# Performance work log

Measured on AMD Instinct MI355X. Metric: run time of the kernel, lower is better.

The kernel has to match this reference:

```python
import jax, jax.numpy as jnp
import numpy as np
from math import sqrt

DIM = 256
HEADS = 4
GROUPS = min(DIM // 4, 32)  # = 32
EPS = 1e-6


def setup_inputs() -> dict:
    key = jax.random.key(0)
    ks = jax.random.split(key, 10)
    B, C, H, W = 16, DIM, 32, 32
    x = jax.random.normal(ks[0], (B, C, H, W), dtype=jnp.float32)
    s = 1.0 / sqrt(C)
    inp = {
        'x': x,
        'gn_scale': jnp.ones((C,), jnp.float32),
        'gn_bias': jnp.zeros((C,), jnp.float32),
        'Wq': jax.random.normal(ks[1], (C, C), jnp.float32) * s,
        'bq': jnp.zeros((C,), jnp.float32),
        'Wk': jax.random.normal(ks[2], (C, C), jnp.float32) * s,
        'bk': jnp.zeros((C,), jnp.float32),
        'Wv': jax.random.normal(ks[3], (C, C), jnp.float32) * s,
        'bv': jnp.zeros((C,), jnp.float32),
        'Wp': jax.random.normal(ks[4], (C, C), jnp.float32) * s,
        'bp': jnp.zeros((C,), jnp.float32),
    }
    return inp


def _group_norm(x, scale, bias):
    B, C, H, W = x.shape
    xg = x.reshape(B, GROUPS, C // GROUPS, H, W)
    mean = xg.mean(axis=(2, 3, 4), keepdims=True)
    var = xg.var(axis=(2, 3, 4), keepdims=True)
    xg = (xg - mean) * jax.lax.rsqrt(var + EPS)
    x = xg.reshape(B, C, H, W)
    return x * scale[None, :, None, None] + bias[None, :, None, None]


def _lin_ch(x, W, b):
    # 1x1 conv / linear over channel dim: (B,C,H,W) x (C,Cout) -> (B,Cout,H,W)
    return jnp.einsum('bchw,cd->bdhw', x, W) + b[None, :, None, None]


def reference(x, gn_scale, gn_bias, Wq, bq, Wk, bk, Wv, bv, Wp, bp):
    B, C, H, W = x.shape
    dh = C // HEADS
    _x = _group_norm(x, gn_scale, gn_bias)
    q = _lin_ch(_x, Wq, bq).reshape(B, HEADS, dh, H, W)
    k = _lin_ch(_x, Wk, bk).reshape(B, HEADS, dh, H, W)
    v = _lin_ch(_x, Wv, bv).reshape(B, HEADS, dh, H, W)
    scores = jnp.einsum('bhdxy,bhdij->bhxyij', q, k) / sqrt(C)
    scores = scores.reshape(B, HEADS, H, W, H * W)
    weights = jax.nn.softmax(scores, axis=-1).reshape(B, HEADS, H, W, H, W)
    h = jnp.einsum('bhxyij,bhdij->bhdxy', weights, v).reshape(B, C, H, W)
    h = _lin_ch(h, Wp, bp)
    ret = (x + h) / sqrt(2.0)
    return ret
```

## Files before the change

### kernel.cpp

```cpp
#include <hip/hip_runtime.h>
#include <hip/hip_bf16.h>

#define BATCH 16
#define CH    256
#define HW    1024
#define NH    4
#define DH    64
#define NG    32
#define CPG   8
#define EPSV  1e-6f

#define QSCALE 0.090168440055558706f

typedef __bf16 bf16x8 __attribute__((ext_vector_type(8)));
typedef float  f32x4  __attribute__((ext_vector_type(4)));

__device__ __forceinline__ unsigned short f2bf(float f) {
    union { __hip_bfloat16 h; unsigned short u; } cv;
    cv.h = __float2bfloat16(f);
    return cv.u;
}

__device__ __forceinline__ unsigned int fbits(float f) {
    union { float f; unsigned int u; } cv; cv.f = f; return cv.u;
}

__device__ __forceinline__ void gld_lds16(const unsigned short* g, unsigned short* l) {
    __builtin_amdgcn_global_load_lds(
        (const __attribute__((address_space(1))) void*)g,
        (__attribute__((address_space(3))) void*)l, 16, 0, 0);
}

__global__ void prep_kernel(const float* Wq, const float* Wk, const float* Wv,
                            const float* Wp, const float* bq, const float* bk,
                            const float* bv, unsigned short* wqkv_t,
                            unsigned short* wp_t, float* bqkv) {
    int idx = blockIdx.x * 256 + threadIdx.x;
    if (idx < 768 * 256) {
        int n = idx >> 8, c = idx & 255;
        const float* W = (n < 256) ? Wq : (n < 512) ? Wk : Wv;
        int d = n & 255;
        wqkv_t[idx] = f2bf(W[c * 256 + d]);
    } else if (idx < 768 * 256 + 256 * 256) {
        int j = idx - 768 * 256;
        int n = j >> 8, c = j & 255;
        wp_t[j] = f2bf(Wp[c * 256 + n]);
    }
    if (idx < 768)
        bqkv[idx] = (idx < 256) ? bq[idx] : (idx < 512) ? bk[idx - 256] : bv[idx - 512];
}

__global__ void gn_stats_kernel(const float* x, const float* scale, const float* bias,
                                float* coefA, float* coefB) {
    int bg = blockIdx.x;
    const float4* p = reinterpret_cast<const float4*>(x + (size_t)bg * (CPG * HW));
    int t = threadIdx.x;
    float s = 0.f, ss = 0.f;
    for (int i = t; i < CPG * HW / 4; i += 256) {
        float4 v = p[i];
        s += v.x + v.y + v.z + v.w;
        ss += v.x * v.x + v.y * v.y + v.z * v.z + v.w * v.w;
    }
    for (int o = 32; o; o >>= 1) { s += __shfl_down(s, o); ss += __shfl_down(ss, o); }
    __shared__ float as[4], ass[4];
    int w = t >> 6;
    if ((t & 63) == 0) { as[w] = s; ass[w] = ss; }
    __syncthreads();
    if (t < 8) {
        float S = as[0] + as[1] + as[2] + as[3];
        float SS = ass[0] + ass[1] + ass[2] + ass[3];
        float mean = S / (float)(CPG * HW);
        float var = SS / (float)(CPG * HW) - mean * mean;
        float rstd = rsqrtf(var + EPSV);
        int b = bg >> 5, g = bg & 31;
        int c = g * CPG + t;
        float a = rstd * scale[c];
        coefA[b * CH + c] = a;
        coefB[b * CH + c] = bias[c] - mean * a;
    }
}

__global__ __launch_bounds__(256) void qkv_kernel(const float* x,
        const float* coefA, const float* coefB,
        const unsigned short* wqkv_t, const float* bqkv,
        unsigned short* qb, unsigned short* kb, unsigned short* vb) {
    int t = threadIdx.x;
    int wv = t >> 6, lane = t & 63, quad = lane >> 4, ln = lane & 15;
    int wr = wv >> 1, wc = wv & 1;
    int bx = blockIdx.x;
    int m0 = bx * 128 + wr * 64;
    int n0 = blockIdx.y * 128 + wc * 64;
    int bb = bx >> 3;
    int p0 = (bx & 7) * 128;

    __shared__ __align__(16) unsigned short lds_a[128][40];

    const float* xb = x + (size_t)bb * CH * HW + p0;
    const float* cA = coefA + bb * CH;
    const float* cB = coefB + bb * CH;

    int sp = t & 127;
    int sbase = (t >> 7) * 2;

    f32x4 acc[4][4] = {};
    for (int k0 = 0; k0 < CH; k0 += 32) {
        bf16x8 wpk[2];
#pragma unroll
        for (int rep = 0; rep < 2; rep++) {
            int s = sbase + rep;
            int cb = k0 + s * 8;
            union { bf16x8 v8; __hip_bfloat162 h2[4]; } u;
#pragma unroll
            for (int j = 0; j < 4; j++) {
                float v0 = fmaf(xb[(size_t)(cb + 2 * j)     * HW + sp], cA[cb + 2 * j],     cB[cb + 2 * j]);
                float v1 = fmaf(xb[(size_t)(cb + 2 * j + 1) * HW + sp], cA[cb + 2 * j + 1], cB[cb + 2 * j + 1]);
                u.h2[j] = __float22bfloat162_rn(float2{v0, v1});
            }
            wpk[rep] = u.v8;
        }
        __syncthreads();
#pragma unroll
        for (int rep = 0; rep < 2; rep++) {
            int s = sbase + rep;
            int phys = s ^ (sp & 3);
            *reinterpret_cast<bf16x8*>(&lds_a[sp][phys * 8]) = wpk[rep];
        }
        __syncthreads();
        bf16x8 af[4], bfr[4];
#pragma unroll
        for (int i = 0; i < 4; i++) {
            int p = wr * 64 + i * 16 + ln;
            af[i] = *reinterpret_cast<const bf16x8*>(&lds_a[p][(quad ^ (p & 3)) * 8]);
        }
#pragma unroll
        for (int j = 0; j < 4; j++)
            bfr[j] = *reinterpret_cast<const bf16x8*>(
                wqkv_t + (size_t)(n0 + j * 16 + ln) * CH + k0 + quad * 8);
#pragma unroll
        for (int i = 0; i < 4; i++)
#pragma unroll
            for (int j = 0; j < 4; j++)
                acc[i][j] = __builtin_amdgcn_mfma_f32_16x16x32_bf16(af[i], bfr[j], acc[i][j], 0, 0, 0);
    }
#pragma unroll
    for (int j = 0; j < 4; j++) {
        int n = n0 + j * 16 + ln;
        float bias = bqkv[n];
        int which = n >> 8;
        int dh_ = n & 255;
        int head = dh_ >> 6, d = dh_ & 63;
#pragma unroll
        for (int i = 0; i < 4; i++) {
            int mb = m0 + i * 16 + quad * 4;
            int bi = mb >> 10, p = mb & 1023;
            int bh = bi * NH + head;
            if (which < 2) {
                unsigned short* dst = (which == 0 ? qb : kb) + (size_t)bh * HW * DH;
                float sc = (which == 0) ? QSCALE : 1.0f;
#pragma unroll
                for (int r = 0; r < 4; r++)
                    dst[(size_t)(p + r) * DH + d] = f2bf((acc[i][j][r] + bias) * sc);
            } else {
                unsigned short* dst = vb + ((size_t)bh * DH + d) * HW + p;
                ushort4 pk4;
                pk4.x = f2bf(acc[i][j][0] + bias);
                pk4.y = f2bf(acc[i][j][1] + bias);
                pk4.z = f2bf(acc[i][j][2] + bias);
                pk4.w = f2bf(acc[i][j][3] + bias);
                *reinterpret_cast<ushort4*>(dst) = pk4;
            }
        }
    }
}

__global__ __launch_bounds__(256) void attn_kernel(const unsigned short* qb,
        const unsigned short* kb, const unsigned short* vb, unsigned short* h_t) {
    int qblk = blockIdx.x, bh = blockIdx.y;
    int t = threadIdx.x;
    int wv = t >> 6, lane = t & 63, quad = lane >> 4, ln = lane & 15;
    int q0 = qblk * 128 + wv * 32;

    const unsigned short* Q = qb + (size_t)bh * HW * DH;
    const unsigned short* K = kb + (size_t)bh * HW * DH;
    const unsigned short* V = vb + (size_t)bh * DH * HW;

    __shared__ __align__(16) unsigned short kbuf[2][4096];
    __shared__ __align__(16) unsigned short vbuf[2][4096];
    __shared__ __align__(16) unsigned short pbuf[4][2][16][72];

    int c_a = wv * 64 + lane;
    int c_b = 256 + wv * 64 + lane;
    int pa = c_a >> 3, ja = (c_a & 7) ^ (pa & 7);
    int pb = c_b >> 3, jb = (c_b & 7) ^ (pb & 7);
    const unsigned short* pka = K + (size_t)pa * DH + ja * 8;
    const unsigned short* pkb = K + (size_t)pb * DH + jb * 8;
    const unsigned short* pva = V + (size_t)pa * HW + ja * 8;
    const unsigned short* pvb = V + (size_t)pb * HW + jb * 8;
    int lofs_a = wv * 512, lofs_b = 2048 + wv * 512;

    int koffs[4][2];
#pragma unroll
    for (int mt = 0; mt < 4; mt++) {
        int p = mt * 16 + ln, sw = p & 7;
#pragma unroll
        for (int kk = 0; kk < 2; kk++)
            koffs[mt][kk] = p * 64 + (((kk * 4 + quad) ^ sw) * 8);
    }

    bf16x8 qf[2][2];
#pragma unroll
    for (int nq = 0; nq < 2; nq++)
#pragma unroll
        for (int kk = 0; kk < 2; kk++)
            qf[nq][kk] = *reinterpret_cast<const bf16x8*>(
                Q + (size_t)(q0 + nq * 16 + ln) * DH + kk * 32 + quad * 8);

    f32x4 ls[2] = {};
    f32x4 o[2][4] = {};

    gld_lds16(pka, &kbuf[0][lofs_a]);
    gld_lds16(pkb, &kbuf[0][lofs_b]);
    gld_lds16(pva, &vbuf[0][lofs_a]);
    gld_lds16(pvb, &vbuf[0][lofs_b]);
    pka += 64 * DH; pkb += 64 * DH; pva += 64; pvb += 64;

#define ATTN_TILE(B, DO_STAGE)                                                      \
    {                                                                               \
        __syncthreads();                                                            \
        if (DO_STAGE) {                                                             \
            gld_lds16(pka, &kbuf[B ^ 1][lofs_a]);                                   \
            gld_lds16(pkb, &kbuf[B ^ 1][lofs_b]);                                   \
            gld_lds16(pva, &vbuf[B ^ 1][lofs_a]);                                   \
            gld_lds16(pvb, &vbuf[B ^ 1][lofs_b]);                                   \
            pka += 64 * DH; pkb += 64 * DH; pva += 64; pvb += 64;                   \
        }                                                                           \
        bf16x8 kf[4][2], vf[4][2];                                                  \
        _Pragma("unroll")                                                           \
        for (int mt = 0; mt < 4; mt++) {                                            \
            _Pragma("unroll")                                                       \
            for (int kk = 0; kk < 2; kk++) {                                        \
                kf[mt][kk] = *reinterpret_cast<const bf16x8*>(&kbuf[B][koffs[mt][kk]]); \
                vf[mt][kk] = *reinterpret_cast<const bf16x8*>(&vbuf[B][koffs[mt][kk]]); \
            }                                                                       \
        }                                                                           \
        f32x4 s[2][4] = {};                                                         \
        _Pragma("unroll")                                                           \
        for (int nq = 0; nq < 2; nq++)                                              \
            _Pragma("unroll")                                                       \
            for (int mt = 0; mt < 4; mt++) {                                        \
                s[nq][mt] = __builtin_amdgcn_mfma_f32_16x16x32_bf16(kf[mt][0], qf[nq][0], s[nq][mt], 0, 0, 0); \
                s[nq][mt] = __builtin_amdgcn_mfma_f32_16x16x32_bf16(kf[mt][1], qf[nq][1], s[nq][mt], 0, 0, 0); \
            }                                                                       \
        _Pragma("unroll")                                                           \
        for (int nq = 0; nq < 2; nq++)                                              \
            _Pragma("unroll")                                                       \
            for (int mt = 0; mt < 4; mt++) {                                        \
                float e0 = __builtin_amdgcn_exp2f(s[nq][mt][0]);                    \
                float e1 = __builtin_amdgcn_exp2f(s[nq][mt][1]);                    \
                float e2 = __builtin_amdgcn_exp2f(s[nq][mt][2]);                    \
                float e3 = __builtin_amdgcn_exp2f(s[nq][mt][3]);                    \
                ls[nq][0] += e0; ls[nq][1] += e1;                                   \
                ls[nq][2] += e2; ls[nq][3] += e3;                                   \
                uint2 pk2;                                                          \
                pk2.x = __builtin_amdgcn_perm(fbits(e1), fbits(e0), 0x07060302u);   \
                pk2.y = __builtin_amdgcn_perm(fbits(e3), fbits(e2), 0x07060302u);   \
                *reinterpret_cast<uint2*>(&pbuf[wv][nq][ln][mt * 16 + quad * 4]) = pk2; \
            }                                                                       \
        _Pragma("unroll")                                                           \
        for (int nq = 0; nq < 2; nq++)                                              \
            _Pragma("unroll")                                                       \
            for (int kk = 0; kk < 2; kk++) {                                        \
                bf16x8 pf = *reinterpret_cast<const bf16x8*>(&pbuf[wv][nq][ln][kk * 32 + quad * 8]); \
                _Pragma("unroll")                                                   \
                for (int mt = 0; mt < 4; mt++)                                      \
                    o[nq][mt] = __builtin_amdgcn_mfma_f32_16x16x32_bf16(vf[mt][kk], pf, o[nq][mt], 0, 0, 0); \
            }                                                                       \
    }

    for (int u = 0; u < 8; u++) {
        ATTN_TILE(0, true)
        ATTN_TILE(1, (u < 7))
    }
#undef ATTN_TILE

    int b_ = bh >> 2, head = bh & 3;
#pragma unroll
    for (int nq = 0; nq < 2; nq++) {
        float lsum = ls[nq][0] + ls[nq][1] + ls[nq][2] + ls[nq][3];
        lsum += __shfl_xor(lsum, 16);
        lsum += __shfl_xor(lsum, 32);
        float inv = 1.0f / lsum;
        unsigned short* dst = h_t + ((size_t)b_ * HW + q0 + nq * 16 + ln) * CH + head * DH;
#pragma unroll
        for (int mt = 0; mt < 4; mt++) {
            ushort4 pk4;
            pk4.x = f2bf(o[nq][mt][0] * inv);
            pk4.y = f2bf(o[nq][mt][1] * inv);
            pk4.z = f2bf(o[nq][mt][2] * inv);
            pk4.w = f2bf(o[nq][mt][3] * inv);
            *reinterpret_cast<ushort4*>(dst + mt * 16 + quad * 4) = pk4;
        }
    }
}

__global__ __launch_bounds__(256) void proj_kernel(const unsigned short* h_t,
        const unsigned short* wp_t, const float* bp, const float* x, float* out) {
    int t = threadIdx.x;
    int wv = t >> 6, lane = t & 63, quad = lane >> 4, ln = lane & 15;
    int wr = wv >> 1, wc = wv & 1;
    int m0 = blockIdx.x * 64 + wr * 32;
    int n0 = blockIdx.y * 128 + wc * 64;

    f32x4 acc[2][4] = {};
    for (int k0 = 0; k0 < CH; k0 += 32) {
        int koff = k0 + quad * 8;
        bf16x8 af[2], bfr[4];
#pragma unroll
        for (int i = 0; i < 2; i++)
            af[i] = *reinterpret_cast<const bf16x8*>(h_t + (size_t)(m0 + i * 16 + ln) * CH + koff);
#pragma unroll
        for (int j = 0; j < 4; j++)
            bfr[j] = *reinterpret_cast<const bf16x8*>(wp_t + (size_t)(n0 + j * 16 + ln) * CH + koff);
#pragma unroll
        for (int i = 0; i < 2; i++)
#pragma unroll
            for (int j = 0; j < 4; j++)
                acc[i][j] = __builtin_amdgcn_mfma_f32_16x16x32_bf16(af[i], bfr[j], acc[i][j], 0, 0, 0);
    }
    const float inv_s2 = 0.70710678118654752440f;
#pragma unroll
    for (int j = 0; j < 4; j++) {
        int n = n0 + j * 16 + ln;
        float bias = bp[n];
#pragma unroll
        for (int i = 0; i < 2; i++) {
            int mb = m0 + i * 16 + quad * 4;
            int bi = mb >> 10, p = mb & 1023;
            size_t off = ((size_t)(bi * CH + n)) * HW + p;
            float4 xv = *reinterpret_cast<const float4*>(x + off);
            float4 ov;
            ov.x = (xv.x + acc[i][j][0] + bias) * inv_s2;
            ov.y = (xv.y + acc[i][j][1] + bias) * inv_s2;
            ov.z = (xv.z + acc[i][j][2] + bias) * inv_s2;
            ov.w = (xv.w + acc[i][j][3] + bias) * inv_s2;
            *reinterpret_cast<float4*>(out + off) = ov;
        }
    }
}

extern "C" void kernel_launch(void* const* d_in, const int* in_sizes, int n_in,
                              void* d_out, int out_size, void* d_ws, size_t ws_size,
                              hipStream_t stream) {
    const float* x        = (const float*)d_in[0];
    const float* gn_scale = (const float*)d_in[1];
    const float* gn_bias  = (const float*)d_in[2];
    const float* Wq = (const float*)d_in[3];
    const float* bq = (const float*)d_in[4];
    const float* Wk = (const float*)d_in[5];
    const float* bk = (const float*)d_in[6];
    const float* Wv = (const float*)d_in[7];
    const float* bv = (const float*)d_in[8];
    const float* Wp = (const float*)d_in[9];
    const float* bp = (const float*)d_in[10];
    float* out = (float*)d_out;

    char* ws = (char*)d_ws;
    float*          bqkv   = (float*)(ws + 0);
    float*          coefA  = (float*)(ws + 4096);
    float*          coefB  = (float*)(ws + 20480);
    unsigned short* wqkv_t = (unsigned short*)(ws + 36864);
    unsigned short* wp_t   = (unsigned short*)(ws + 430080);
    unsigned short* h_t    = (unsigned short*)(ws + 1048576);
    unsigned short* qb     = (unsigned short*)(ws + 9437184);
    unsigned short* kb     = (unsigned short*)(ws + 17825792);
    unsigned short* vb     = (unsigned short*)(ws + 26214400);

    prep_kernel<<<1024, 256, 0, stream>>>(Wq, Wk, Wv, Wp, bq, bk, bv, wqkv_t, wp_t, bqkv);
    gn_stats_kernel<<<512, 256, 0, stream>>>(x, gn_scale, gn_bias, coefA, coefB);
    qkv_kernel<<<dim3(128, 6), 256, 0, stream>>>(x, coefA, coefB, wqkv_t, bqkv, qb, kb, vb);
    attn_kernel<<<dim3(8, 64), 256, 0, stream>>>(qb, kb, vb, h_t);
    proj_kernel<<<dim3(256, 2), 256, 0, stream>>>(h_t, wp_t, bp, x, out);
}
```

Before: 163.0 us.

## Merge prep and GN-stats kernels, retile QKV GEMM with prefetch, add MFMA priority

Folds the weight-conversion and group-norm statistics kernels into a single launch to save one kernel launch. Retiles the QKV GEMM to 64x256 block tiles, where each thread stages one 8-channel slot and prefetches the next slice of x into registers, with launch bounds requesting 3 blocks per SIMD. Wraps the attention MFMA sections in s_setprio so matrix-core work gets issue priority. The mix trades register pressure and smaller M tiles for fewer launches and better latency hiding.

After: 172.9 us. 6.0% more time.

```diff
diff --git a/kernel.cpp b/kernel.cpp
--- a/kernel.cpp
+++ b/kernel.cpp
@@ -31,56 +31,57 @@
         (__attribute__((address_space(3))) void*)l, 16, 0, 0);
 }
 
-__global__ void prep_kernel(const float* Wq, const float* Wk, const float* Wv,
-                            const float* Wp, const float* bq, const float* bk,
-                            const float* bv, unsigned short* wqkv_t,
-                            unsigned short* wp_t, float* bqkv) {
-    int idx = blockIdx.x * 256 + threadIdx.x;
-    if (idx < 768 * 256) {
-        int n = idx >> 8, c = idx & 255;
-        const float* W = (n < 256) ? Wq : (n < 512) ? Wk : Wv;
-        int d = n & 255;
-        wqkv_t[idx] = f2bf(W[c * 256 + d]);
-    } else if (idx < 768 * 256 + 256 * 256) {
-        int j = idx - 768 * 256;
-        int n = j >> 8, c = j & 255;
-        wp_t[j] = f2bf(Wp[c * 256 + n]);
-    }
-    if (idx < 768)
-        bqkv[idx] = (idx < 256) ? bq[idx] : (idx < 512) ? bk[idx - 256] : bv[idx - 512];
-}
-
-__global__ void gn_stats_kernel(const float* x, const float* scale, const float* bias,
-                                float* coefA, float* coefB) {
-    int bg = blockIdx.x;
-    const float4* p = reinterpret_cast<const float4*>(x + (size_t)bg * (CPG * HW));
+__global__ void prep_gn_kernel(const float* Wq, const float* Wk, const float* Wv,
+                               const float* Wp, const float* bq, const float* bk,
+                               const float* bv, unsigned short* wqkv_t,
+                               unsigned short* wp_t, float* bqkv,
+                               const float* x, const float* scale, const float* bias,
+                               float* coefA, float* coefB) {
     int t = threadIdx.x;
-    float s = 0.f, ss = 0.f;
-    for (int i = t; i < CPG * HW / 4; i += 256) {
-        float4 v = p[i];
-        s += v.x + v.y + v.z + v.w;
-        ss += v.x * v.x + v.y * v.y + v.z * v.z + v.w * v.w;
-    }
-    for (int o = 32; o; o >>= 1) { s += __shfl_down(s, o); ss += __shfl_down(ss, o); }
-    __shared__ float as[4], ass[4];
-    int w = t >> 6;
-    if ((t & 63) == 0) { as[w] = s; ass[w] = ss; }
-    __syncthreads();
-    if (t < 8) {
-        float S = as[0] + as[1] + as[2] + as[3];
-        float SS = ass[0] + ass[1] + ass[2] + ass[3];
-        float mean = S / (float)(CPG * HW);
-        float var = SS / (float)(CPG * HW) - mean * mean;
-        float rstd = rsqrtf(var + EPSV);
-        int b = bg >> 5, g = bg & 31;
-        int c = g * CPG + t;
-        float a = rstd * scale[c];
-        coefA[b * CH + c] = a;
-        coefB[b * CH + c] = bias[c] - mean * a;
-    }
-}
-
-__global__ __launch_bounds__(256) void qkv_kernel(const float* x,
+    if (blockIdx.x < 1024) {
+        int idx = blockIdx.x * 256 + t;
+        if (idx < 768 * 256) {
+            int n = idx >> 8, c = idx & 255;
+            const float* W = (n < 256) ? Wq : (n < 512) ? Wk : Wv;
+            int d = n & 255;
+            wqkv_t[idx] = f2bf(W[c * 256 + d]);
+        } else {
+            int j = idx - 768 * 256;
+            int n = j >> 8, c = j & 255;
+            wp_t[j] = f2bf(Wp[c * 256 + n]);
+        }
+        if (idx < 768)
+            bqkv[idx] = (idx < 256) ? bq[idx] : (idx < 512) ? bk[idx - 256] : bv[idx - 512];
+    } else {
+        int bg = blockIdx.x - 1024;
+        const float4* p = reinterpret_cast<const float4*>(x + (size_t)bg * (CPG * HW));
+        float s = 0.f, ss = 0.f;
+        for (int i = t; i < CPG * HW / 4; i += 256) {
+            float4 v = p[i];
+            s += v.x + v.y + v.z + v.w;
+            ss += v.x * v.x + v.y * v.y + v.z * v.z + v.w * v.w;
+        }
+        for (int o = 32; o; o >>= 1) { s += __shfl_down(s, o); ss += __shfl_down(ss, o); }
+        __shared__ float as_[4], ass_[4];
+        int w = t >> 6;
+        if ((t & 63) == 0) { as_[w] = s; ass_[w] = ss; }
+        __syncthreads();
+        if (t < 8) {
+            float S = as_[0] + as_[1] + as_[2] + as_[3];
+            float SS = ass_[0] + ass_[1] + ass_[2] + ass_[3];
+            float mean = S / (float)(CPG * HW);
+            float var = SS / (float)(CPG * HW) - mean * mean;
+            float rstd = rsqrtf(var + EPSV);
+            int b = bg >> 5, g = bg & 31;
+            int c = g * CPG + t;
+            float a = rstd * scale[c];
+            coefA[b * CH + c] = a;
+            coefB[b * CH + c] = bias[c] - mean * a;
+        }
+    }
+}
+
+__global__ __launch_bounds__(256, 3) void qkv_kernel(const float* x,
         const float* coefA, const float* coefB,
         const unsigned short* wqkv_t, const float* bqkv,
         unsigned short* qb, unsigned short* kb, unsigned short* vb) {
@@ -88,69 +89,70 @@
     int wv = t >> 6, lane = t & 63, quad = lane >> 4, ln = lane & 15;
     int wr = wv >> 1, wc = wv & 1;
     int bx = blockIdx.x;
-    int m0 = bx * 128 + wr * 64;
-    int n0 = blockIdx.y * 128 + wc * 64;
-    int bb = bx >> 3;
-    int p0 = (bx & 7) * 128;
-
-    __shared__ __align__(16) unsigned short lds_a[128][40];
+    int m0 = bx * 64 + wr * 32;
+    int n0 = blockIdx.y * 256 + wc * 128;
+    int bb = bx >> 4;
+    int p0 = (bx & 15) * 64;
+
+    __shared__ __align__(16) unsigned short lds_a[64][40];
 
     const float* xb = x + (size_t)bb * CH * HW + p0;
     const float* cA = coefA + bb * CH;
     const float* cB = coefB + bb * CH;
 
-    int sp = t & 127;
-    int sbase = (t >> 7) * 2;
-
-    f32x4 acc[4][4] = {};
+    int sp = t & 63;
+    int slot = t >> 6;
+
+    float xv[8];
+#pragma unroll
+    for (int j = 0; j < 8; j++)
+        xv[j] = xb[(size_t)(slot * 8 + j) * HW + sp];
+
+    f32x4 acc[2][8] = {};
     for (int k0 = 0; k0 < CH; k0 += 32) {
-        bf16x8 wpk[2];
-#pragma unroll
-        for (int rep = 0; rep < 2; rep++) {
-            int s = sbase + rep;
-            int cb = k0 + s * 8;
-            union { bf16x8 v8; __hip_bfloat162 h2[4]; } u;
-#pragma unroll
-            for (int j = 0; j < 4; j++) {
-                float v0 = fmaf(xb[(size_t)(cb + 2 * j)     * HW + sp], cA[cb + 2 * j],     cB[cb + 2 * j]);
-                float v1 = fmaf(xb[(size_t)(cb + 2 * j + 1) * HW + sp], cA[cb + 2 * j + 1], cB[cb + 2 * j + 1]);
-                u.h2[j] = __float22bfloat162_rn(float2{v0, v1});
-            }
-            wpk[rep] = u.v8;
-        }
-        __syncthreads();
-#pragma unroll
-        for (int rep = 0; rep < 2; rep++) {
-            int s = sbase + rep;
-            int phys = s ^ (sp & 3);
-            *reinterpret_cast<bf16x8*>(&lds_a[sp][phys * 8]) = wpk[rep];
-        }
-        __syncthreads();
-        bf16x8 af[4], bfr[4];
-#pragma unroll
-        for (int i = 0; i < 4; i++) {
-            int p = wr * 64 + i * 16 + ln;
-            af[i] = *reinterpret_cast<const bf16x8*>(&lds_a[p][(quad ^ (p & 3)) * 8]);
-        }
-#pragma unroll
-        for (int j = 0; j < 4; j++)
+        int cb = k0 + slot * 8;
+        union { bf16x8 v8; __hip_bfloat162 h2[4]; } u;
+#pragma unroll
+        for (int j = 0; j < 4; j++) {
+            float v0 = fmaf(xv[2 * j],     cA[cb + 2 * j],     cB[cb + 2 * j]);
+            float v1 = fmaf(xv[2 * j + 1], cA[cb + 2 * j + 1], cB[cb + 2 * j + 1]);
+            u.h2[j] = __float22bfloat162_rn(float2{v0, v1});
+        }
+        if (k0 + 32 < CH) {
+#pragma unroll
+            for (int j = 0; j < 8; j++)
+                xv[j] = xb[(size_t)(cb + 32 + j) * HW + sp];
+        }
+        bf16x8 bfr[8];
+#pragma unroll
+        for (int j = 0; j < 8; j++)
             bfr[j] = *reinterpret_cast<const bf16x8*>(
                 wqkv_t + (size_t)(n0 + j * 16 + ln) * CH + k0 + quad * 8);
-#pragma unroll
-        for (int i = 0; i < 4; i++)
-#pragma unroll
-            for (int j = 0; j < 4; j++)
+        __syncthreads();
+        int phys = slot ^ (sp & 3);
+        *reinterpret_cast<bf16x8*>(&lds_a[sp][phys * 8]) = u.v8;
+        __syncthreads();
+        bf16x8 af[2];
+#pragma unroll
+        for (int i = 0; i < 2; i++) {
+            int p = wr * 32 + i * 16 + ln;
+            af[i] = *reinterpret_cast<const bf16x8*>(&lds_a[p][(quad ^ (p & 3)) * 8]);
+        }
+#pragma unroll
+        for (int i = 0; i < 2; i++)
+#pragma unroll
+            for (int j = 0; j < 8; j++)
                 acc[i][j] = __builtin_amdgcn_mfma_f32_16x16x32_bf16(af[i], bfr[j], acc[i][j], 0, 0, 0);
     }
 #pragma unroll
-    for (int j = 0; j < 4; j++) {
+    for (int j = 0; j < 8; j++) {
         int n = n0 + j * 16 + ln;
         float bias = bqkv[n];
         int which = n >> 8;
         int dh_ = n & 255;
         int head = dh_ >> 6, d = dh_ & 63;
 #pragma unroll
-        for (int i = 0; i < 4; i++) {
+        for (int i = 0; i < 2; i++) {
             int mb = m0 + i * 16 + quad * 4;
             int bi = mb >> 10, p = mb & 1023;
             int bh = bi * NH + head;
@@ -244,6 +246,7 @@
             }                                                                       \
         }                                                                           \
         f32x4 s[2][4] = {};                                                         \
+        __builtin_amdgcn_s_setprio(1);                                              \
         _Pragma("unroll")                                                           \
         for (int nq = 0; nq < 2; nq++)                                              \
             _Pragma("unroll")                                                       \
@@ -251,6 +254,7 @@
                 s[nq][mt] = __builtin_amdgcn_mfma_f32_16x16x32_bf16(kf[mt][0], qf[nq][0], s[nq][mt], 0, 0, 0); \
                 s[nq][mt] = __builtin_amdgcn_mfma_f32_16x16x32_bf16(kf[mt][1], qf[nq][1], s[nq][mt], 0, 0, 0); \
             }                                                                       \
+        __builtin_amdgcn_s_setprio(0);                                              \
         _Pragma("unroll")                                                           \
         for (int nq = 0; nq < 2; nq++)                                              \
             _Pragma("unroll")                                                       \
@@ -271,9 +275,11 @@
             _Pragma("unroll")                                                       \
             for (int kk = 0; kk < 2; kk++) {                                        \
                 bf16x8 pf = *reinterpret_cast<const bf16x8*>(&pbuf[wv][nq][ln][kk * 32 + quad * 8]); \
+                __builtin_amdgcn_s_setprio(1);                                      \
                 _Pragma("unroll")                                                   \
                 for (int mt = 0; mt < 4; mt++)                                      \
                     o[nq][mt] = __builtin_amdgcn_mfma_f32_16x16x32_bf16(vf[mt][kk], pf, o[nq][mt], 0, 0, 0); \
+                __builtin_amdgcn_s_setprio(0);                                      \
             }                                                                       \
     }
 
@@ -375,9 +381,10 @@
     unsigned short* kb     = (unsigned short*)(ws + 17825792);
     unsigned short* vb     = (unsigned short*)(ws + 26214400);
 
-    prep_kernel<<<1024, 256, 0, stream>>>(Wq, Wk, Wv, Wp, bq, bk, bv, wqkv_t, wp_t, bqkv);
-    gn_stats_kernel<<<512, 256, 0, stream>>>(x, gn_scale, gn_bias, coefA, coefB);
-    qkv_kernel<<<dim3(128, 6), 256, 0, stream>>>(x, coefA, coefB, wqkv_t, bqkv, qb, kb, vb);
+    prep_gn_kernel<<<1536, 256, 0, stream>>>(Wq, Wk, Wv, Wp, bq, bk, bv,
+                                             wqkv_t, wp_t, bqkv,
+                                             x, gn_scale, gn_bias, coefA, coefB);
+    qkv_kernel<<<dim3(256, 3), 256, 0, stream>>>(x, coefA, coefB, wqkv_t, bqkv, qb, kb, vb);
     attn_kernel<<<dim3(8, 64), 256, 0, stream>>>(qb, kb, vb, h_t);
     proj_kernel<<<dim3(256, 2), 256, 0, stream>>>(h_t, wp_t, bp, x, out);
 }
```
